# Optimization experiments

Hardware: AMD Instinct MI355X
Metric: run time of the kernel (lower is better)

The kernel has to match this reference:

```python
import jax, jax.numpy as jnp
import numpy as np

TAU_RC = 0.02
TAU_REF = 0.002
V_TH = 1.0
EPS = 1e-7


def lif_rate(I):
    # LIF firing-rate nonlinearity: r = 1/(tau_ref - tau_rc*log1p(-v_th/I)) for I > v_th+eps else 0
    good = I > V_TH + EPS
    safe_I = jnp.where(good, I, V_TH + 1.0)  # avoid log1p of invalid values
    r = 1.0 / (TAU_REF - TAU_RC * jnp.log1p(-V_TH / safe_I))
    return jnp.where(good, r, 0.0)


def setup_inputs() -> dict:
    key = jax.random.key(0)
    kq, kk, kv, ke, kg, kb = jax.random.split(key, 6)
    B, H, T, D = 2, 16, 2048, 64
    block_size = 2048
    Q = jax.random.normal(kq, (B, H, T, D), dtype=jnp.float32)
    K = jax.random.normal(kk, (B, H, T, D), dtype=jnp.float32)
    V = jax.random.normal(kv, (B, H, T, D), dtype=jnp.float32)
    enc = jax.random.normal(ke, (H, block_size, D), dtype=jnp.float32)
    # F.normalize(enc, dim=-1, eps=1e-8): x / max(||x||, eps)
    norm = jnp.maximum(jnp.linalg.norm(enc, axis=-1, keepdims=True), 1e-8)
    enc_hat = enc / norm
    gain = jax.random.uniform(kg, (1, H, block_size, 1), dtype=jnp.float32) * 200.0
    bias = jax.random.uniform(kb, (1, H, block_size, 1), dtype=jnp.float32)
    return {"Q": Q, "K": K, "V": V, "enc_hat": enc_hat, "gain": gain, "bias": bias}


def reference(Q, K, V, enc_hat, gain, bias):
    B, H, T, D = Q.shape
    temperature = jnp.asarray(D ** 0.5, dtype=Q.dtype)
    E = enc_hat[:, :T, :]          # [H, T, D]
    G = gain[:, :, :T, :]          # [1, H, T, 1]
    BIAS = bias[:, :, :T, :]       # [1, H, T, 1]
    # scores against fixed encoders (K is unused, matching the original module)
    I = G * jnp.einsum('bhtd,hsd->bhts', Q, E) + BIAS   # [B, H, T, T]
    scores = lif_rate(I) / temperature
    causal = jnp.tril(jnp.ones((T, T), dtype=bool))[None, None]
    scores = jnp.where(causal, scores, -jnp.inf)
    attn = jax.nn.softmax(scores, axis=-1)
    return jnp.einsum('bhts,bhsd->bhtd', attn, V)
```

## Files before the change

### kernel.cpp

```cpp
#include <hip/hip_runtime.h>
#include <hip/hip_bf16.h>
#include <math.h>

constexpr int Bb = 2, Hh = 16, Tt = 2048;

typedef __attribute__((ext_vector_type(8))) _Float16 f16x8;
typedef __attribute__((ext_vector_type(8))) short bf16x8;
typedef __attribute__((ext_vector_type(4))) float f32x4;
typedef __attribute__((ext_vector_type(16))) float f32x16;
typedef __attribute__((ext_vector_type(4))) unsigned int u32x4;
typedef unsigned int u32;

__device__ __forceinline__ short f2bf(float x){ __hip_bfloat16 h = __float2bfloat16(x); return *(short*)&h; }
__device__ __forceinline__ int swze(int row, int e){ return row*64 + ((((e>>3) ^ (row&7))<<3) | (e&7)); }
__device__ __forceinline__ int swzg(int row, int e0){ return row*64 + ((((e0>>3) ^ (row&7))<<3)); }

__device__ __forceinline__ void gll16(const void* g, void* l){
  __builtin_amdgcn_global_load_lds((const __attribute__((address_space(1))) u32*)g,
                                   (__attribute__((address_space(3))) u32*)l, 16, 0, 0);
}
__device__ __forceinline__ u32 cvtpk(float lo, float hi){
  u32 d; asm("v_cvt_pk_bf16_f32 %0, %1, %2" : "=v"(d) : "v"(lo), "v"(hi)); return d;
}

__global__ __launch_bounds__(256) void prep_e(const float* __restrict__ E, char* __restrict__ Eimg){
  const float* src = E + (size_t)blockIdx.x * 4096;
  char* dst = Eimg + (size_t)blockIdx.x * 16384;
#pragma unroll
  for (int i = 0; i < 2; ++i) {
    const int gid = threadIdx.x + 256 * i;
    const int row = gid >> 3, gc = gid & 7;
    const float* s8 = src + row * 64 + gc * 8;
    float4 a = *(const float4*)s8;
    float4 c = *(const float4*)(s8 + 4);
    float v[8] = {a.x, a.y, a.z, a.w, c.x, c.y, c.z, c.w};
    f16x8 hv, lv;
#pragma unroll
    for (int k = 0; k < 8; ++k) {
      _Float16 hi = (_Float16)v[k];
      hv[k] = hi; lv[k] = (_Float16)(v[k] - (float)hi);
    }
    const int off = row * 128 + ((gc ^ (row & 7)) << 4);
    *(f16x8*)(dst + off) = hv;
    *(f16x8*)(dst + 8192 + off) = lv;
  }
}

__global__ __launch_bounds__(256) void prep_v(const float* __restrict__ V, char* __restrict__ Vimg){
  __shared__ __align__(16) short Tl[64 * 64];
  const int tid = threadIdx.x;
  const int j = blockIdx.x & 31, bh = blockIdx.x >> 5;
  const int s0 = j * 64;
  {
    const int r = tid >> 2, c0 = (tid & 3) * 16;
    const float* src = V + ((size_t)bh * Tt + s0 + r) * 64 + c0;
#pragma unroll
    for (int i = 0; i < 4; ++i) {
      float4 t4 = ((const float4*)src)[i];
      float vv[4] = {t4.x, t4.y, t4.z, t4.w};
#pragma unroll
      for (int k = 0; k < 4; ++k) Tl[swze(c0 + 4 * i + k, r)] = f2bf(vv[k]);
    }
  }
  __syncthreads();
  {
    const int d = tid >> 2, sg = (tid & 3) * 16;
    bf16x8 a = *(const bf16x8*)&Tl[swzg(d, sg)];
    bf16x8 b = *(const bf16x8*)&Tl[swzg(d, sg + 8)];
    char* dst = Vimg + (size_t)blockIdx.x * 8192;
    *(bf16x8*)(dst + (sg >> 3) * 1024 + d * 16)       = a;
    *(bf16x8*)(dst + ((sg >> 3) + 1) * 1024 + d * 16) = b;
  }
}

__global__ __launch_bounds__(256, 2) void lif_attn10(
    const float* __restrict__ Q, const float* __restrict__ gain, const float* __restrict__ bias,
    const char* __restrict__ Eimg, const char* __restrict__ Vimg, float* __restrict__ out)
{
  __shared__ __align__(16) char Eb[2][16384];
  __shared__ __align__(16) float LsS[128];

  const int tid = threadIdx.x, lane = tid & 63;
  const int l31 = lane & 31, hi2 = lane >> 5;
  const int w = tid >> 6, wc = w & 1, wr = w >> 1;
  const int bh = blockIdx.x & 31, pairp = blockIdx.x >> 5;
  const int b = bh >> 4, h = bh & 15;

  const char* etile = Eimg + (size_t)(h * 32) * 16384;
  const char* vtile = Vimg + (size_t)(bh * 32) * 8192;

  const int rS = 32 * wr + l31;
  const int eB = rS * 128 + ((hi2 ^ (rS & 7)) << 4);
  const int g8a = 4 * wr + hi2;
  const char* vp0 = vtile + g8a * 1024 + l31 * 16;
  const char* vp1 = vtile + g8a * 1024 + (32 + l31) * 16;
  const char* vp2 = vtile + (g8a + 2) * 1024 + l31 * 16;
  const char* vp3 = vtile + (g8a + 2) * 1024 + (32 + l31) * 16;

  for (int ph = 0; ph < 2; ++ph) {
    const int tb = ph ? (31 - pairp) : pairp;
    const int t0 = tb * 64;
    const int tg = t0 + 32 * wc + l31;

    f16x8 qh[4], ql[4];
    {
      const float* qp = Q + ((size_t)(b * Hh + h) * Tt + tg) * 64 + 8 * hi2;
#pragma unroll
      for (int kk = 0; kk < 4; ++kk) {
        const float* p0 = qp + 16 * kk;
        float4 a = *(const float4*)p0;
        float4 c = *(const float4*)(p0 + 4);
        float v[8] = {a.x, a.y, a.z, a.w, c.x, c.y, c.z, c.w};
#pragma unroll
        for (int k = 0; k < 8; ++k) {
          _Float16 hi = (_Float16)v[k];
          qh[kk][k] = hi; ql[kk][k] = (_Float16)(v[k] - (float)hi);
        }
      }
    }
    const float gt = gain[h * Tt + tg], bt = bias[h * Tt + tg];

    f32x16 oacc0 = 0.f, oacc1 = 0.f;
    float lsum = 0.f;
    f32x16 sA, sB;
    bf16x8 vA[4], vB[4];

    auto STAGE_E = [&](int n, int buf) {
      const char* g = etile + (size_t)n * 16384 + tid * 16;
      char* l = &Eb[buf][0] + tid * 16;
#pragma unroll
      for (int c2 = 0; c2 < 4; ++c2) gll16(g + c2 * 4096, l + c2 * 4096);
    };
    auto SSTEP = [&](int buf, f32x16& acc) {
      const char* ec = &Eb[buf][0];
      acc = 0.f;
      __builtin_amdgcn_s_setprio(1);
#pragma unroll
      for (int kk = 0; kk < 4; ++kk) {
        f16x8 eh = *(const f16x8*)(ec + (eB ^ (kk << 5)));
        f16x8 el = *(const f16x8*)(ec + 8192 + (eB ^ (kk << 5)));
        acc = __builtin_amdgcn_mfma_f32_32x32x16_f16(eh, qh[kk], acc, 0, 0, 0);
        acc = __builtin_amdgcn_mfma_f32_32x32x16_f16(el, qh[kk], acc, 0, 0, 0);
        acc = __builtin_amdgcn_mfma_f32_32x32x16_f16(eh, ql[kk], acc, 0, 0, 0);
      }
      __builtin_amdgcn_s_setprio(0);
    };
    auto VLOAD = [&](int n, bf16x8* vv) {
      const size_t o = (size_t)n * 8192;
      vv[0] = *(const bf16x8*)(vp0 + o);
      vv[1] = *(const bf16x8*)(vp1 + o);
      vv[2] = *(const bf16x8*)(vp2 + o);
      vv[3] = *(const bf16x8*)(vp3 + o);
    };

    auto BODY = [&](int j, f32x16& cur, f32x16& nxt, bf16x8* vc, bf16x8* vn) {
      if (j + 2 <= tb) STAGE_E(j + 2, j & 1);
      __builtin_amdgcn_sched_barrier(0);
      if (j + 1 <= tb) { SSTEP((j + 1) & 1, nxt); VLOAD(j + 1, vn); }
      float p[16];
#pragma unroll
      for (int r = 0; r < 16; ++r) {
        const float I = fmaf(gt, cur[r], bt);
        const float a = (I - 1.0f) * __builtin_fabsf(__builtin_amdgcn_rcpf(I));
        const float L2 = __log2f(a);
        const float den = fmaf(-0.013862944f, L2, 0.002f);
        const float rd = __builtin_amdgcn_rcpf(den);
        const float pv = __builtin_amdgcn_exp2f(fmaf(0.18033688f, rd, -90.169312f));
        p[r] = fmaxf(pv, 7.1892351e-28f);
      }
      if (j == tb) {
#pragma unroll
        for (int rq = 0; rq < 4; ++rq)
#pragma unroll
          for (int rr = 0; rr < 4; ++rr)
            if (32 * wr + 8 * rq + 4 * hi2 + rr > 32 * wc + l31) p[4 * rq + rr] = 0.f;
      }
#pragma unroll
      for (int r = 0; r < 16; ++r) lsum += p[r];
      __builtin_amdgcn_s_setprio(1);
#pragma unroll
      for (int kp = 0; kp < 2; ++kp) {
        u32 x0 = cvtpk(p[8 * kp + 0], p[8 * kp + 1]);
        u32 x1 = cvtpk(p[8 * kp + 2], p[8 * kp + 3]);
        u32 y0 = cvtpk(p[8 * kp + 4], p[8 * kp + 5]);
        u32 y1 = cvtpk(p[8 * kp + 6], p[8 * kp + 7]);
        asm("v_permlane32_swap_b32 %0, %1" : "+v"(x0), "+v"(y0));
        asm("v_permlane32_swap_b32 %0, %1" : "+v"(x1), "+v"(y1));
        u32x4 af = {x0, x1, y0, y1};
        bf16x8 pa = *(bf16x8*)&af;
        oacc0 = __builtin_amdgcn_mfma_f32_32x32x16_bf16(pa, vc[2 * kp + 0], oacc0, 0, 0, 0);
        oacc1 = __builtin_amdgcn_mfma_f32_32x32x16_bf16(pa, vc[2 * kp + 1], oacc1, 0, 0, 0);
      }
      __builtin_amdgcn_s_setprio(0);
    };

    STAGE_E(0, 0);
    if (tb >= 1) STAGE_E(1, 1);
    __builtin_amdgcn_sched_barrier(0);
    VLOAD(0, vA);
    asm volatile("s_waitcnt vmcnt(4)" ::: "memory");
    __builtin_amdgcn_s_barrier();
    __builtin_amdgcn_sched_barrier(0);
    SSTEP(0, sA);
    asm volatile("s_waitcnt vmcnt(4)" ::: "memory");
    __builtin_amdgcn_s_barrier();
    __builtin_amdgcn_sched_barrier(0);

    int j = 0;
    for (;;) {
      BODY(j, sA, sB, vA, vB);
      if (j == tb) break;
      asm volatile("s_waitcnt vmcnt(4)" ::: "memory");
      __builtin_amdgcn_s_barrier();
      __builtin_amdgcn_sched_barrier(0);
      ++j;
      BODY(j, sB, sA, vB, vA);
      if (j == tb) break;
      asm volatile("s_waitcnt vmcnt(4)" ::: "memory");
      __builtin_amdgcn_s_barrier();
      __builtin_amdgcn_sched_barrier(0);
      ++j;
    }

    lsum += __shfl_xor(lsum, 32);
    if (lane < 32) LsS[wr * 64 + wc * 32 + l31] = lsum;
    __syncthreads();
    float* red = (float*)&Eb[0][0];
    if (wr == 1) {
#pragma unroll
      for (int rq = 0; rq < 4; ++rq)
#pragma unroll
        for (int rr = 0; rr < 4; ++rr) {
          const int tr = 8 * rq + 4 * hi2 + rr;
          red[wc * 2048 + tr * 64 + l31]      = oacc0[4 * rq + rr];
          red[wc * 2048 + tr * 64 + 32 + l31] = oacc1[4 * rq + rr];
        }
    }
    __syncthreads();
    if (wr == 0) {
      float* ob = out + ((size_t)(b * Hh + h) * Tt + t0 + 32 * wc) * 64;
#pragma unroll
      for (int rq = 0; rq < 4; ++rq) {
        const int tr0 = 8 * rq + 4 * hi2;
        f32x4 lt0 = *(const f32x4*)&LsS[wc * 32 + tr0];
        f32x4 lt1 = *(const f32x4*)&LsS[64 + wc * 32 + tr0];
#pragma unroll
        for (int rr = 0; rr < 4; ++rr) {
          const int tr = tr0 + rr;
          const float linv = __builtin_amdgcn_rcpf(lt0[rr] + lt1[rr]);
          const float o0 = oacc0[4 * rq + rr] + red[wc * 2048 + tr * 64 + l31];
          const float o1 = oacc1[4 * rq + rr] + red[wc * 2048 + tr * 64 + 32 + l31];
          ob[(size_t)tr * 64 + l31]      = o0 * linv;
          ob[(size_t)tr * 64 + 32 + l31] = o1 * linv;
        }
      }
    }
    __syncthreads();
  }
}

extern "C" void kernel_launch(void* const* d_in, const int* in_sizes, int n_in,
                              void* d_out, int out_size, void* d_ws, size_t ws_size,
                              hipStream_t stream) {
  const float* Q    = (const float*)d_in[0];
  const float* V    = (const float*)d_in[2];
  const float* E    = (const float*)d_in[3];
  const float* gain = (const float*)d_in[4];
  const float* bias = (const float*)d_in[5];
  float* out = (float*)d_out;

  constexpr size_t EIMG_BYTES = (size_t)Hh * 32 * 16384;
  char* Eimg = (char*)d_ws;
  char* Vimg = (char*)d_ws + EIMG_BYTES;

  prep_e<<<Hh * 32, 256, 0, stream>>>(E, Eimg);
  prep_v<<<Bb * Hh * 32, 256, 0, stream>>>(V, Vimg);
  lif_attn10<<<512, 256, 0, stream>>>(Q, gain, bias, Eimg, Vimg, out);
}
```

Baseline: 77.63 us.

## Give each wave private LDS E staging to drop block-wide barriers

New measurement: 77.90 us. No clear change (+0.3%).

```diff
diff --git a/kernel.cpp b/kernel.cpp
--- a/kernel.cpp
+++ b/kernel.cpp
@@ -73,11 +73,11 @@
   }
 }
 
-__global__ __launch_bounds__(256, 2) void lif_attn10(
+__global__ __launch_bounds__(256, 2) void lif_attn13(
     const float* __restrict__ Q, const float* __restrict__ gain, const float* __restrict__ bias,
     const char* __restrict__ Eimg, const char* __restrict__ Vimg, float* __restrict__ out)
 {
-  __shared__ __align__(16) char Eb[2][16384];
+  __shared__ __align__(16) char Eb[4][2][8192];
   __shared__ __align__(16) float LsS[128];
 
   const int tid = threadIdx.x, lane = tid & 63;
@@ -89,8 +89,10 @@
   const char* etile = Eimg + (size_t)(h * 32) * 16384;
   const char* vtile = Vimg + (size_t)(bh * 32) * 8192;
 
-  const int rS = 32 * wr + l31;
-  const int eB = rS * 128 + ((hi2 ^ (rS & 7)) << 4);
+  char* Ebp = &Eb[w][0][0];
+
+  const int eBp = l31 * 128 + ((hi2 ^ (l31 & 7)) << 4);
+
   const int g8a = 4 * wr + hi2;
   const char* vp0 = vtile + g8a * 1024 + l31 * 16;
   const char* vp1 = vtile + g8a * 1024 + (32 + l31) * 16;
@@ -126,19 +128,22 @@
     bf16x8 vA[4], vB[4];
 
     auto STAGE_E = [&](int n, int buf) {
-      const char* g = etile + (size_t)n * 16384 + tid * 16;
-      char* l = &Eb[buf][0] + tid * 16;
-#pragma unroll
-      for (int c2 = 0; c2 < 4; ++c2) gll16(g + c2 * 4096, l + c2 * 4096);
+      const char* g = etile + (size_t)n * 16384 + wr * 4096 + lane * 16;
+      char* l = Ebp + buf * 8192 + lane * 16;
+#pragma unroll
+      for (int c2 = 0; c2 < 4; ++c2) {
+        gll16(g + c2 * 1024, l + c2 * 1024);
+        gll16(g + 8192 + c2 * 1024, l + 4096 + c2 * 1024);
+      }
     };
     auto SSTEP = [&](int buf, f32x16& acc) {
-      const char* ec = &Eb[buf][0];
+      const char* ec = Ebp + buf * 8192;
       acc = 0.f;
       __builtin_amdgcn_s_setprio(1);
 #pragma unroll
       for (int kk = 0; kk < 4; ++kk) {
-        f16x8 eh = *(const f16x8*)(ec + (eB ^ (kk << 5)));
-        f16x8 el = *(const f16x8*)(ec + 8192 + (eB ^ (kk << 5)));
+        f16x8 eh = *(const f16x8*)(ec + (eBp ^ (kk << 5)));
+        f16x8 el = *(const f16x8*)(ec + 4096 + (eBp ^ (kk << 5)));
         acc = __builtin_amdgcn_mfma_f32_32x32x16_f16(eh, qh[kk], acc, 0, 0, 0);
         acc = __builtin_amdgcn_mfma_f32_32x32x16_f16(el, qh[kk], acc, 0, 0, 0);
         acc = __builtin_amdgcn_mfma_f32_32x32x16_f16(eh, ql[kk], acc, 0, 0, 0);
@@ -156,7 +161,14 @@
     auto BODY = [&](int j, f32x16& cur, f32x16& nxt, bf16x8* vc, bf16x8* vn) {
       if (j + 2 <= tb) STAGE_E(j + 2, j & 1);
       __builtin_amdgcn_sched_barrier(0);
-      if (j + 1 <= tb) { SSTEP((j + 1) & 1, nxt); VLOAD(j + 1, vn); }
+      if (j + 1 <= tb) {
+        VLOAD(j + 1, vn);
+        __builtin_amdgcn_sched_barrier(0);
+        if (j + 2 <= tb) { asm volatile("s_waitcnt vmcnt(12)" ::: "memory"); }
+        else             { asm volatile("s_waitcnt vmcnt(4)"  ::: "memory"); }
+        __builtin_amdgcn_sched_barrier(0);
+        SSTEP((j + 1) & 1, nxt);
+      }
       float p[16];
 #pragma unroll
       for (int r = 0; r < 16; ++r) {
@@ -198,34 +210,22 @@
     if (tb >= 1) STAGE_E(1, 1);
     __builtin_amdgcn_sched_barrier(0);
     VLOAD(0, vA);
-    asm volatile("s_waitcnt vmcnt(4)" ::: "memory");
-    __builtin_amdgcn_s_barrier();
+    __builtin_amdgcn_sched_barrier(0);
+    if (tb >= 1) { asm volatile("s_waitcnt vmcnt(12)" ::: "memory"); }
+    else         { asm volatile("s_waitcnt vmcnt(4)"  ::: "memory"); }
     __builtin_amdgcn_sched_barrier(0);
     SSTEP(0, sA);
-    asm volatile("s_waitcnt vmcnt(4)" ::: "memory");
-    __builtin_amdgcn_s_barrier();
-    __builtin_amdgcn_sched_barrier(0);
 
     int j = 0;
     for (;;) {
-      BODY(j, sA, sB, vA, vB);
-      if (j == tb) break;
-      asm volatile("s_waitcnt vmcnt(4)" ::: "memory");
-      __builtin_amdgcn_s_barrier();
-      __builtin_amdgcn_sched_barrier(0);
-      ++j;
-      BODY(j, sB, sA, vB, vA);
-      if (j == tb) break;
-      asm volatile("s_waitcnt vmcnt(4)" ::: "memory");
-      __builtin_amdgcn_s_barrier();
-      __builtin_amdgcn_sched_barrier(0);
-      ++j;
+      BODY(j, sA, sB, vA, vB); if (j == tb) break; ++j;
+      BODY(j, sB, sA, vB, vA); if (j == tb) break; ++j;
     }
 
     lsum += __shfl_xor(lsum, 32);
     if (lane < 32) LsS[wr * 64 + wc * 32 + l31] = lsum;
     __syncthreads();
-    float* red = (float*)&Eb[0][0];
+    float* red = (float*)&Eb[0][0][0];
     if (wr == 1) {
 #pragma unroll
       for (int rq = 0; rq < 4; ++rq)
@@ -275,5 +275,5 @@
 
   prep_e<<<Hh * 32, 256, 0, stream>>>(E, Eimg);
   prep_v<<<Bb * Hh * 32, 256, 0, stream>>>(V, Vimg);
-  lif_attn10<<<512, 256, 0, stream>>>(Q, gain, bias, Eimg, Vimg, out);
-}
+  lif_attn13<<<512, 256, 0, stream>>>(Q, gain, bias, Eimg, Vimg, out);
+}
```
